# Kernel optimization log

Hardware: AMD Instinct MI355X
Metric: run time of the kernel (lower is better)

## Reference

```python
import jax, jax.numpy as jnp
import numpy as np

N_HEAD = 12
LN_EPS = 1e-5


def setup_inputs() -> dict:
    key = jax.random.key(0)
    ks = jax.random.split(key, 4)
    B, T, C = 4, 2048, 768
    s = C ** -0.5
    return {
        "x": jax.random.normal(ks[0], (B, T, C), jnp.float32),
        "w_attn": jax.random.normal(ks[1], (C, 3 * C), jnp.float32) * s,
        "b_attn": jnp.zeros((3 * C,), jnp.float32),
        "w_proj": jax.random.normal(ks[2], (C, C), jnp.float32) * s,
        "b_proj": jnp.zeros((C,), jnp.float32),
        "ln1_g": jnp.ones((C,), jnp.float32),
        "ln1_b": jnp.zeros((C,), jnp.float32),
        "ln2_g": jnp.ones((C,), jnp.float32),
        "ln2_b": jnp.zeros((C,), jnp.float32),
    }


def _layernorm(x, g, b):
    mu = jnp.mean(x, axis=-1, keepdims=True)
    var = jnp.mean(jnp.square(x - mu), axis=-1, keepdims=True)
    return (x - mu) * jax.lax.rsqrt(var + LN_EPS) * g + b


def _attn(h, w_attn, b_attn, w_proj, b_proj):
    B, T, C = h.shape
    hd = C // N_HEAD
    # Faithful to torch: view(B,T,H,3*hd) then split 3*hd -> q,k,v per head
    qkv = (h @ w_attn + b_attn).reshape(B, T, N_HEAD, 3, hd)
    q = jnp.transpose(qkv[:, :, :, 0, :], (0, 2, 1, 3))  # (B,H,T,hd)
    k = jnp.transpose(qkv[:, :, :, 1, :], (0, 2, 1, 3))
    v = jnp.transpose(qkv[:, :, :, 2, :], (0, 2, 1, 3))
    # NOTE: scale is C**-0.5 (full embed dim) and there is NO causal mask,
    # exactly as in the source.
    scores = jnp.einsum("bhtd,bhsd->bhts", q, k) * (C ** -0.5)
    a = jax.nn.softmax(scores, axis=-1)
    y = jnp.einsum("bhts,bhsd->bhtd", a, v)
    y = jnp.transpose(y, (0, 2, 1, 3)).reshape(B, T, C)
    return y @ w_proj + b_proj


def reference(x, w_attn, b_attn, w_proj, b_proj, ln1_g, ln1_b, ln2_g, ln2_b):
    # Faithful to source Block.forward: attn applied twice, MLP never called.
    x = x + _attn(_layernorm(x, ln1_g, ln1_b), w_attn, b_attn, w_proj, b_proj)
    x = x + _attn(_layernorm(x, ln2_g, ln2_b), w_attn, b_attn, w_proj, b_proj)
    return x
```

## Files before the change

### kernel.cpp

```cpp
#include <hip/hip_runtime.h>


using bf16x8 = __attribute__((ext_vector_type(8))) short;
using f32x4  = __attribute__((ext_vector_type(4))) float;
using f32x16 = __attribute__((ext_vector_type(16))) float;

__device__ __forceinline__ unsigned short f2b(float f) {
  unsigned u = __builtin_bit_cast(unsigned, f);
  u += 0x7FFFu + ((u >> 16) & 1u);
  return (unsigned short)(u >> 16);
}
__device__ __forceinline__ unsigned pk2(float a, float b) {
  unsigned ua = __builtin_bit_cast(unsigned, a);
  ua += 0x7FFFu + ((ua >> 16) & 1u);
  unsigned ub = __builtin_bit_cast(unsigned, b);
  ub += 0x7FFFu + ((ub >> 16) & 1u);
  return (ua >> 16) | (ub & 0xFFFF0000u);
}

__device__ __forceinline__ bf16x8 mk8(unsigned a, unsigned b, unsigned c,
                                      unsigned d) {
  union { unsigned u[4]; bf16x8 v; } x;
  x.u[0] = a; x.u[1] = b; x.u[2] = c; x.u[3] = d;
  return x.v;
}

#define ASYNC16(g, l)                                                        \
  __builtin_amdgcn_global_load_lds(                                          \
      (const __attribute__((address_space(1))) void*)(g),                    \
      (__attribute__((address_space(3))) void*)(l), 16, 0, 0)

#define PLSWAP(a, b) asm("v_permlane32_swap_b32 %0, %1" : "+v"(a), "+v"(b))

__global__ __launch_bounds__(256) void wt_kernel(const float* __restrict__ w,
                                                 unsigned short* __restrict__ wt,
                                                 int N) {
  __shared__ float tile[32][33];
  const int n0 = blockIdx.x * 32, k0 = blockIdx.y * 32;
  const int tx = threadIdx.x, ty = threadIdx.y;
#pragma unroll
  for (int i = 0; i < 32; i += 8)
    tile[ty + i][tx] = w[(size_t)(k0 + ty + i) * N + n0 + tx];
  __syncthreads();
#pragma unroll
  for (int i = 0; i < 32; i += 8)
    wt[(size_t)(n0 + ty + i) * 768 + k0 + tx] = f2b(tile[tx][ty + i]);
}

__global__ __launch_bounds__(256) void ln_kernel(const float* __restrict__ x,
                                                 const float* __restrict__ g,
                                                 const float* __restrict__ b,
                                                 unsigned short* __restrict__ h) {
  __shared__ float red[8];
  const int row = blockIdx.x;
  const int tid = threadIdx.x;
  const float* xr = x + (size_t)row * 768;
  float v0 = xr[tid], v1 = xr[tid + 256], v2 = xr[tid + 512];
  float s = v0 + v1 + v2;
  float s2 = v0 * v0 + v1 * v1 + v2 * v2;
#pragma unroll
  for (int off = 1; off < 64; off <<= 1) {
    s += __shfl_xor(s, off);
    s2 += __shfl_xor(s2, off);
  }
  if ((tid & 63) == 0) { red[tid >> 6] = s; red[4 + (tid >> 6)] = s2; }
  __syncthreads();
  const float S  = red[0] + red[1] + red[2] + red[3];
  const float S2 = red[4] + red[5] + red[6] + red[7];
  const float mu  = S * (1.0f / 768.0f);
  const float var = S2 * (1.0f / 768.0f) - mu * mu;
  const float inv = rsqrtf(var + 1e-5f);
  unsigned short* hr = h + (size_t)row * 768;
  hr[tid]       = f2b((v0 - mu) * inv * g[tid] + b[tid]);
  hr[tid + 256] = f2b((v1 - mu) * inv * g[tid + 256] + b[tid + 256]);
  hr[tid + 512] = f2b((v2 - mu) * inv * g[tid + 512] + b[tid + 512]);
}

template <int EPI>
__global__ __launch_bounds__(256, 2) void gemm_kernel(
    const unsigned short* __restrict__ A, const unsigned short* __restrict__ Bt,
    const float* __restrict__ bias, const float* __restrict__ resid,
    unsigned short* __restrict__ q, unsigned short* __restrict__ k,
    unsigned short* __restrict__ vt, float* __restrict__ outF) {
  __shared__ alignas(16) unsigned short As[128 * 32];
  __shared__ alignas(16) unsigned short Bs[128 * 32];

  const int tid = threadIdx.x;
  const int wv = tid >> 6;
  const int lane = tid & 63;
  const int quad = lane >> 4;
  const int l15 = lane & 15;
  const int m0 = blockIdx.y * 128;
  const int n0 = blockIdx.x * 128;

  const int o0 = wv * 1024 + lane * 16;
  const int rT0 = o0 >> 6, c0 = (o0 & 63) >> 1;
  const int o1 = o0 + 4096;
  const int rT1 = o1 >> 6, c1 = (o1 & 63) >> 1;

  const unsigned short* gA0 = A + (size_t)(m0 + rT0) * 768 + c0;
  const unsigned short* gA1 = A + (size_t)(m0 + rT1) * 768 + c1;
  const unsigned short* gB0 = Bt + (size_t)(n0 + rT0) * 768 + c0;
  const unsigned short* gB1 = Bt + (size_t)(n0 + rT1) * 768 + c1;
  unsigned short* lA0 = &As[wv * 512];
  unsigned short* lA1 = &As[wv * 512 + 2048];
  unsigned short* lB0 = &Bs[wv * 512];
  unsigned short* lB1 = &Bs[wv * 512 + 2048];

  f32x4 acc[4][4];
#pragma unroll
  for (int i = 0; i < 4; ++i)
#pragma unroll
    for (int j = 0; j < 4; ++j) acc[i][j] = {0.f, 0.f, 0.f, 0.f};

  const int mBase = (wv >> 1) * 64;
  const int nBase = (wv & 1) * 64;

  for (int kk = 0; kk < 24; ++kk) {
    const int ko = kk * 32;
    ASYNC16(gA0 + ko, lA0);
    ASYNC16(gA1 + ko, lA1);
    ASYNC16(gB0 + ko, lB0);
    ASYNC16(gB1 + ko, lB1);
    __syncthreads();
    bf16x8 af[4], bfv[4];
#pragma unroll
    for (int mt = 0; mt < 4; ++mt)
      af[mt] = *(const bf16x8*)&As[(mBase + mt * 16 + l15) * 32 + quad * 8];
#pragma unroll
    for (int nt = 0; nt < 4; ++nt)
      bfv[nt] = *(const bf16x8*)&Bs[(nBase + nt * 16 + l15) * 32 + quad * 8];
#pragma unroll
    for (int mt = 0; mt < 4; ++mt)
#pragma unroll
      for (int nt = 0; nt < 4; ++nt)
        acc[mt][nt] = __builtin_amdgcn_mfma_f32_16x16x32_bf16(af[mt], bfv[nt],
                                                              acc[mt][nt], 0, 0, 0);
    __syncthreads();
  }

  if constexpr (EPI == 0) {
    const float c2 = 0.052062786090587f;
#pragma unroll
    for (int mt = 0; mt < 4; ++mt) {
#pragma unroll
      for (int nt = 0; nt < 4; ++nt) {
        const int n = n0 + nBase + nt * 16 + l15;
        const int head = n / 192;
        const int rem = n - head * 192;
        const int sel = rem >> 6;
        const int d = rem & 63;
        const float bv = bias[n];
        const int mr = m0 + mBase + mt * 16 + quad * 4;
        const int bb = mr >> 11;
        const int t = mr & 2047;
        if (sel == 2) {
          const unsigned long long pk =
              (unsigned long long)pk2(acc[mt][nt][0] + bv, acc[mt][nt][1] + bv) |
              ((unsigned long long)pk2(acc[mt][nt][2] + bv, acc[mt][nt][3] + bv) << 32);
          *(unsigned long long*)&vt[(((size_t)bb * 12 + head) * 64 + d) * 2048 + t] = pk;
        } else {
          unsigned short* tgt = (sel == 0) ? q : k;
          const float sc = (sel == 0) ? c2 : 1.0f;
#pragma unroll
          for (int r = 0; r < 4; ++r)
            tgt[(((size_t)bb * 12 + head) * 2048 + t + r) * 64 + d] =
                f2b((acc[mt][nt][r] + bv) * sc);
        }
      }
    }
  } else {
#pragma unroll
    for (int mt = 0; mt < 4; ++mt) {
#pragma unroll
      for (int nt = 0; nt < 4; ++nt) {
        const int n = n0 + nBase + nt * 16 + l15;
        const float bv = bias[n];
#pragma unroll
        for (int r = 0; r < 4; ++r) {
          const int m = m0 + mBase + mt * 16 + quad * 4 + r;
          const size_t idx = (size_t)m * 768 + n;
          outF[idx] = resid[idx] + bv + acc[mt][nt][r];
        }
      }
    }
  }
}

__global__ __launch_bounds__(256, 3) void attn_kernel(
    const unsigned short* __restrict__ Q, const unsigned short* __restrict__ Km,
    const unsigned short* __restrict__ Vt, unsigned short* __restrict__ Y) {
  __shared__ alignas(16) unsigned short Ks[2][64 * 64];
  __shared__ alignas(16) unsigned short Vs[2][64 * 64];

  const int bh   = blockIdx.x;
  const int qt   = blockIdx.y;
  const int tid  = threadIdx.x;
  const int wv   = tid >> 6;
  const int lane = tid & 63;
  const int l31  = lane & 31;
  const int hi   = lane >> 5;
  const int s7   = l31 & 7;
  const size_t bhT = (size_t)bh * 2048;

  bf16x8 qf[4];
  {
    const unsigned short* qb =
        Q + (bhT + qt * 128 + wv * 32 + l31) * 64 + hi * 8;
#pragma unroll
    for (int ks = 0; ks < 4; ++ks) qf[ks] = *(const bf16x8*)(qb + ks * 16);
  }

  const int L0 = wv * 1024 + (lane << 4);
  const int L1 = L0 + 4096;
  const int r0 = L0 >> 7, b0 = (L0 & 127) ^ ((r0 & 7) << 4);
  const int r1 = L1 >> 7, b1 = (L1 & 127) ^ ((r1 & 7) << 4);
  const unsigned short* kg0 = Km + (bhT + r0) * 64 + (b0 >> 1);
  const unsigned short* kg1 = Km + (bhT + r1) * 64 + (b1 >> 1);
  const unsigned short* vg0 = Vt + ((size_t)bh * 64 + r0) * 2048 + (b0 >> 1);
  const unsigned short* vg1 = Vt + ((size_t)bh * 64 + r1) * 2048 + (b1 >> 1);
  const int kb0 = wv * 512, kb1 = wv * 512 + 2048;

  f32x16 o0, o1;
#pragma unroll
  for (int i = 0; i < 16; ++i) { o0[i] = 0.f; o1[i] = 0.f; }
  float l_acc = 0.f;

  ASYNC16(kg0, &Ks[0][kb0]);
  ASYNC16(kg1, &Ks[0][kb1]);
  ASYNC16(vg0, &Vs[0][kb0]);
  ASYNC16(vg1, &Vs[0][kb1]);
  __syncthreads();

  for (int c = 0; c < 32; ++c) {
    const int p = c & 1;
    if (c < 31) {
      const int ka = (c + 1) * 4096, va = (c + 1) * 64;
      ASYNC16(kg0 + ka, &Ks[p ^ 1][kb0]);
      ASYNC16(kg1 + ka, &Ks[p ^ 1][kb1]);
      ASYNC16(vg0 + va, &Vs[p ^ 1][kb0]);
      ASYNC16(vg1 + va, &Vs[p ^ 1][kb1]);
    }
    const unsigned short* Kp = &Ks[p][0];
    const unsigned short* Vp = &Vs[p][0];

#pragma unroll
    for (int tt = 0; tt < 2; ++tt) {
      f32x16 s;
#pragma unroll
      for (int i = 0; i < 16; ++i) s[i] = 0.f;
#pragma unroll
      for (int ks = 0; ks < 4; ++ks) {
        const int off = tt * 4096 + l31 * 128 + (((ks * 2 + hi) ^ s7) << 4);
        bf16x8 kf = *(const bf16x8*)&Kp[off >> 1];
        s = __builtin_amdgcn_mfma_f32_32x32x16_bf16(kf, qf[ks], s, 0, 0, 0);
      }

      unsigned dw[8];
      float lc = 0.f;
#pragma unroll
      for (int r2 = 0; r2 < 8; ++r2) {
        const float e0 = __builtin_amdgcn_exp2f(s[2 * r2]);
        const float e1 = __builtin_amdgcn_exp2f(s[2 * r2 + 1]);
        const unsigned u0 = __builtin_bit_cast(unsigned, e0) & 0xFFFF0000u;
        const unsigned u1 = __builtin_bit_cast(unsigned, e1) & 0xFFFF0000u;
        lc += __builtin_bit_cast(float, u0) + __builtin_bit_cast(float, u1);
        dw[r2] = (u0 >> 16) | u1;
      }
      l_acc += lc;

      PLSWAP(dw[0], dw[2]);
      PLSWAP(dw[1], dw[3]);
      PLSWAP(dw[4], dw[6]);
      PLSWAP(dw[5], dw[7]);
      const bf16x8 pf0 = mk8(dw[0], dw[1], dw[2], dw[3]);
      const bf16x8 pf1 = mk8(dw[4], dw[5], dw[6], dw[7]);

#pragma unroll
      for (int dt = 0; dt < 2; ++dt) {
        const int vb = dt * 4096 + l31 * 128;
        const int kv0 = tt * 2, kv1 = tt * 2 + 1;
        bf16x8 vf0 = *(const bf16x8*)&Vp[(vb + (((kv0 * 2 + hi) ^ s7) << 4)) >> 1];
        bf16x8 vf1 = *(const bf16x8*)&Vp[(vb + (((kv1 * 2 + hi) ^ s7) << 4)) >> 1];
        if (dt == 0) {
          o0 = __builtin_amdgcn_mfma_f32_32x32x16_bf16(vf0, pf0, o0, 0, 0, 0);
          o0 = __builtin_amdgcn_mfma_f32_32x32x16_bf16(vf1, pf1, o0, 0, 0, 0);
        } else {
          o1 = __builtin_amdgcn_mfma_f32_32x32x16_bf16(vf0, pf0, o1, 0, 0, 0);
          o1 = __builtin_amdgcn_mfma_f32_32x32x16_bf16(vf1, pf1, o1, 0, 0, 0);
        }
      }
    }
    __syncthreads();
  }

  unsigned la = __builtin_bit_cast(unsigned, l_acc), lb = la;
  PLSWAP(la, lb);
  const float l_tot =
      l_acc + __builtin_bit_cast(float, hi ? la : lb);
  const float rl = 1.0f / l_tot;

  const int b = bh / 12;
  const int head = bh - b * 12;
  const int row = qt * 128 + wv * 32 + l31;
  unsigned short* yb = Y + ((size_t)(b * 2048 + row)) * 768 + head * 64;
#pragma unroll
  for (int dt = 0; dt < 2; ++dt) {
#pragma unroll
    for (int g4 = 0; g4 < 4; ++g4) {
      const int d = dt * 32 + g4 * 8 + hi * 4;
      const float a0 = (dt ? o1[g4 * 4 + 0] : o0[g4 * 4 + 0]) * rl;
      const float a1 = (dt ? o1[g4 * 4 + 1] : o0[g4 * 4 + 1]) * rl;
      const float a2 = (dt ? o1[g4 * 4 + 2] : o0[g4 * 4 + 2]) * rl;
      const float a3 = (dt ? o1[g4 * 4 + 3] : o0[g4 * 4 + 3]) * rl;
      const unsigned long long pk =
          (unsigned long long)pk2(a0, a1) | ((unsigned long long)pk2(a2, a3) << 32);
      *(unsigned long long*)(yb + d) = pk;
    }
  }
}

extern "C" void kernel_launch(void* const* d_in, const int* in_sizes, int n_in,
                              void* d_out, int out_size, void* d_ws, size_t ws_size,
                              hipStream_t stream) {
  const float* x      = (const float*)d_in[0];
  const float* w_attn = (const float*)d_in[1];
  const float* b_attn = (const float*)d_in[2];
  const float* w_proj = (const float*)d_in[3];
  const float* b_proj = (const float*)d_in[4];
  const float* ln_g[2] = {(const float*)d_in[5], (const float*)d_in[7]};
  const float* ln_b[2] = {(const float*)d_in[6], (const float*)d_in[8]};
  float* out = (float*)d_out;

  unsigned short* wAt = (unsigned short*)d_ws;
  unsigned short* wPt = wAt + 2304 * 768;
  unsigned short* h   = wPt + 768 * 768;
  unsigned short* q   = h + 8192 * 768;
  unsigned short* k   = q + 48 * 2048 * 64;
  unsigned short* vt  = k + 48 * 2048 * 64;
  unsigned short* y   = vt + 48 * 2048 * 64;

  wt_kernel<<<dim3(72, 24), dim3(32, 8), 0, stream>>>(w_attn, wAt, 2304);
  wt_kernel<<<dim3(24, 24), dim3(32, 8), 0, stream>>>(w_proj, wPt, 768);

  for (int pass = 0; pass < 2; ++pass) {
    const float* xin = pass ? (const float*)out : x;
    ln_kernel<<<8192, 256, 0, stream>>>(xin, ln_g[pass], ln_b[pass], h);
    gemm_kernel<0><<<dim3(18, 64), 256, 0, stream>>>(h, wAt, b_attn, nullptr,
                                                     q, k, vt, nullptr);
    attn_kernel<<<dim3(48, 16), 256, 0, stream>>>(q, k, vt, y);
    gemm_kernel<1><<<dim3(6, 64), 256, 0, stream>>>(y, wPt, b_proj, xin,
                                                    nullptr, nullptr, nullptr, out);
  }
}
```

Measured before the change: 386.6 us.

## Give each attention wave 64 query rows and stage K/V via registers into padded LDS

The attention kernel now runs 128 threads per block, and each wave processes two 32-row query tiles, so every K and V fragment read from LDS feeds twice as many MFMAs. The direct-to-LDS async copies and XOR swizzle are replaced by global loads into registers, which are written to a padded LDS layout after compute to overlap with the math. MFMA sections are wrapped in s_setprio. This raises register pressure and halves the waves per block. The padded stride also leaves 16-byte LDS accesses only 8-byte aligned, which may cause bank conflicts or split accesses.

```diff
diff --git a/kernel.cpp b/kernel.cpp
--- a/kernel.cpp
+++ b/kernel.cpp
@@ -187,11 +187,12 @@
   }
 }
 
-__global__ __launch_bounds__(256, 3) void attn_kernel(
+#define KPAD 68
+__global__ __launch_bounds__(128, 2) void attn_kernel(
     const unsigned short* __restrict__ Q, const unsigned short* __restrict__ Km,
     const unsigned short* __restrict__ Vt, unsigned short* __restrict__ Y) {
-  __shared__ alignas(16) unsigned short Ks[2][64 * 64];
-  __shared__ alignas(16) unsigned short Vs[2][64 * 64];
+  __shared__ alignas(16) unsigned short Ks[2][64 * KPAD];
+  __shared__ alignas(16) unsigned short Vs[2][64 * KPAD];
 
   const int bh   = blockIdx.x;
   const int qt   = blockIdx.y;
@@ -200,122 +201,158 @@
   const int lane = tid & 63;
   const int l31  = lane & 31;
   const int hi   = lane >> 5;
-  const int s7   = l31 & 7;
   const size_t bhT = (size_t)bh * 2048;
 
-  bf16x8 qf[4];
+  bf16x8 qf0[4], qf1[4];
   {
-    const unsigned short* qb =
-        Q + (bhT + qt * 128 + wv * 32 + l31) * 64 + hi * 8;
-#pragma unroll
-    for (int ks = 0; ks < 4; ++ks) qf[ks] = *(const bf16x8*)(qb + ks * 16);
-  }
-
-  const int L0 = wv * 1024 + (lane << 4);
-  const int L1 = L0 + 4096;
-  const int r0 = L0 >> 7, b0 = (L0 & 127) ^ ((r0 & 7) << 4);
-  const int r1 = L1 >> 7, b1 = (L1 & 127) ^ ((r1 & 7) << 4);
-  const unsigned short* kg0 = Km + (bhT + r0) * 64 + (b0 >> 1);
-  const unsigned short* kg1 = Km + (bhT + r1) * 64 + (b1 >> 1);
-  const unsigned short* vg0 = Vt + ((size_t)bh * 64 + r0) * 2048 + (b0 >> 1);
-  const unsigned short* vg1 = Vt + ((size_t)bh * 64 + r1) * 2048 + (b1 >> 1);
-  const int kb0 = wv * 512, kb1 = wv * 512 + 2048;
-
-  f32x16 o0, o1;
-#pragma unroll
-  for (int i = 0; i < 16; ++i) { o0[i] = 0.f; o1[i] = 0.f; }
-  float l_acc = 0.f;
-
-  ASYNC16(kg0, &Ks[0][kb0]);
-  ASYNC16(kg1, &Ks[0][kb1]);
-  ASYNC16(vg0, &Vs[0][kb0]);
-  ASYNC16(vg1, &Vs[0][kb1]);
+    const unsigned short* qa =
+        Q + (bhT + qt * 128 + wv * 64 + l31) * 64 + hi * 8;
+#pragma unroll
+    for (int ks = 0; ks < 4; ++ks) {
+      qf0[ks] = *(const bf16x8*)(qa + ks * 16);
+      qf1[ks] = *(const bf16x8*)(qa + 32 * 64 + ks * 16);
+    }
+  }
+
+  const int sr = tid >> 1;
+  const int sh = tid & 1;
+  const unsigned short* gK = Km + (bhT + sr) * 64 + sh * 32;
+  const unsigned short* gV = Vt + ((size_t)bh * 64 + sr) * 2048 + sh * 32;
+  const int lofs = sr * KPAD + sh * 32;
+
+  f32x16 o00, o01, o10, o11;
+#pragma unroll
+  for (int i = 0; i < 16; ++i) { o00[i] = 0.f; o01[i] = 0.f; o10[i] = 0.f; o11[i] = 0.f; }
+  float l0 = 0.f, l1 = 0.f;
+
+  bf16x8 kst[4], vst[4];
+#pragma unroll
+  for (int i = 0; i < 4; ++i) {
+    kst[i] = *(const bf16x8*)(gK + i * 8);
+    vst[i] = *(const bf16x8*)(gV + i * 8);
+  }
+#pragma unroll
+  for (int i = 0; i < 4; ++i) {
+    *(bf16x8*)&Ks[0][lofs + i * 8] = kst[i];
+    *(bf16x8*)&Vs[0][lofs + i * 8] = vst[i];
+  }
   __syncthreads();
 
   for (int c = 0; c < 32; ++c) {
     const int p = c & 1;
     if (c < 31) {
-      const int ka = (c + 1) * 4096, va = (c + 1) * 64;
-      ASYNC16(kg0 + ka, &Ks[p ^ 1][kb0]);
-      ASYNC16(kg1 + ka, &Ks[p ^ 1][kb1]);
-      ASYNC16(vg0 + va, &Vs[p ^ 1][kb0]);
-      ASYNC16(vg1 + va, &Vs[p ^ 1][kb1]);
+      const unsigned short* gKn = gK + (size_t)(c + 1) * 4096;
+      const unsigned short* gVn = gV + (c + 1) * 64;
+#pragma unroll
+      for (int i = 0; i < 4; ++i) {
+        kst[i] = *(const bf16x8*)(gKn + i * 8);
+        vst[i] = *(const bf16x8*)(gVn + i * 8);
+      }
     }
     const unsigned short* Kp = &Ks[p][0];
     const unsigned short* Vp = &Vs[p][0];
 
 #pragma unroll
     for (int tt = 0; tt < 2; ++tt) {
-      f32x16 s;
-#pragma unroll
-      for (int i = 0; i < 16; ++i) s[i] = 0.f;
+      bf16x8 kf[4];
+#pragma unroll
+      for (int ks = 0; ks < 4; ++ks)
+        kf[ks] = *(const bf16x8*)&Kp[(tt * 32 + l31) * KPAD + ks * 16 + hi * 8];
+
+      f32x16 s0, s1;
+#pragma unroll
+      for (int i = 0; i < 16; ++i) { s0[i] = 0.f; s1[i] = 0.f; }
+      __builtin_amdgcn_s_setprio(1);
 #pragma unroll
       for (int ks = 0; ks < 4; ++ks) {
-        const int off = tt * 4096 + l31 * 128 + (((ks * 2 + hi) ^ s7) << 4);
-        bf16x8 kf = *(const bf16x8*)&Kp[off >> 1];
-        s = __builtin_amdgcn_mfma_f32_32x32x16_bf16(kf, qf[ks], s, 0, 0, 0);
-      }
-
-      unsigned dw[8];
-      float lc = 0.f;
-#pragma unroll
-      for (int r2 = 0; r2 < 8; ++r2) {
-        const float e0 = __builtin_amdgcn_exp2f(s[2 * r2]);
-        const float e1 = __builtin_amdgcn_exp2f(s[2 * r2 + 1]);
-        const unsigned u0 = __builtin_bit_cast(unsigned, e0) & 0xFFFF0000u;
-        const unsigned u1 = __builtin_bit_cast(unsigned, e1) & 0xFFFF0000u;
-        lc += __builtin_bit_cast(float, u0) + __builtin_bit_cast(float, u1);
-        dw[r2] = (u0 >> 16) | u1;
-      }
-      l_acc += lc;
-
-      PLSWAP(dw[0], dw[2]);
-      PLSWAP(dw[1], dw[3]);
-      PLSWAP(dw[4], dw[6]);
-      PLSWAP(dw[5], dw[7]);
-      const bf16x8 pf0 = mk8(dw[0], dw[1], dw[2], dw[3]);
-      const bf16x8 pf1 = mk8(dw[4], dw[5], dw[6], dw[7]);
-
-#pragma unroll
-      for (int dt = 0; dt < 2; ++dt) {
-        const int vb = dt * 4096 + l31 * 128;
-        const int kv0 = tt * 2, kv1 = tt * 2 + 1;
-        bf16x8 vf0 = *(const bf16x8*)&Vp[(vb + (((kv0 * 2 + hi) ^ s7) << 4)) >> 1];
-        bf16x8 vf1 = *(const bf16x8*)&Vp[(vb + (((kv1 * 2 + hi) ^ s7) << 4)) >> 1];
-        if (dt == 0) {
-          o0 = __builtin_amdgcn_mfma_f32_32x32x16_bf16(vf0, pf0, o0, 0, 0, 0);
-          o0 = __builtin_amdgcn_mfma_f32_32x32x16_bf16(vf1, pf1, o0, 0, 0, 0);
-        } else {
-          o1 = __builtin_amdgcn_mfma_f32_32x32x16_bf16(vf0, pf0, o1, 0, 0, 0);
-          o1 = __builtin_amdgcn_mfma_f32_32x32x16_bf16(vf1, pf1, o1, 0, 0, 0);
+        s0 = __builtin_amdgcn_mfma_f32_32x32x16_bf16(kf[ks], qf0[ks], s0, 0, 0, 0);
+        s1 = __builtin_amdgcn_mfma_f32_32x32x16_bf16(kf[ks], qf1[ks], s1, 0, 0, 0);
+      }
+      __builtin_amdgcn_s_setprio(0);
+
+      unsigned dwa[8], dwb[8];
+      {
+        float lc0 = 0.f, lc1 = 0.f;
+#pragma unroll
+        for (int r2 = 0; r2 < 8; ++r2) {
+          const float a0 = __builtin_amdgcn_exp2f(s0[2 * r2]);
+          const float a1 = __builtin_amdgcn_exp2f(s0[2 * r2 + 1]);
+          const unsigned ua0 = __builtin_bit_cast(unsigned, a0) & 0xFFFF0000u;
+          const unsigned ua1 = __builtin_bit_cast(unsigned, a1) & 0xFFFF0000u;
+          lc0 += __builtin_bit_cast(float, ua0) + __builtin_bit_cast(float, ua1);
+          dwa[r2] = (ua0 >> 16) | ua1;
+          const float b0 = __builtin_amdgcn_exp2f(s1[2 * r2]);
+          const float b1 = __builtin_amdgcn_exp2f(s1[2 * r2 + 1]);
+          const unsigned ub0 = __builtin_bit_cast(unsigned, b0) & 0xFFFF0000u;
+          const unsigned ub1 = __builtin_bit_cast(unsigned, b1) & 0xFFFF0000u;
+          lc1 += __builtin_bit_cast(float, ub0) + __builtin_bit_cast(float, ub1);
+          dwb[r2] = (ub0 >> 16) | ub1;
         }
+        l0 += lc0;
+        l1 += lc1;
+      }
+
+      PLSWAP(dwa[0], dwa[2]); PLSWAP(dwa[1], dwa[3]);
+      PLSWAP(dwa[4], dwa[6]); PLSWAP(dwa[5], dwa[7]);
+      PLSWAP(dwb[0], dwb[2]); PLSWAP(dwb[1], dwb[3]);
+      PLSWAP(dwb[4], dwb[6]); PLSWAP(dwb[5], dwb[7]);
+      const bf16x8 p0a = mk8(dwa[0], dwa[1], dwa[2], dwa[3]);
+      const bf16x8 p0b = mk8(dwa[4], dwa[5], dwa[6], dwa[7]);
+      const bf16x8 p1a = mk8(dwb[0], dwb[1], dwb[2], dwb[3]);
+      const bf16x8 p1b = mk8(dwb[4], dwb[5], dwb[6], dwb[7]);
+
+      bf16x8 v0a = *(const bf16x8*)&Vp[(l31) * KPAD + (tt * 2 + 0) * 16 + hi * 8];
+      bf16x8 v0b = *(const bf16x8*)&Vp[(l31) * KPAD + (tt * 2 + 1) * 16 + hi * 8];
+      bf16x8 v1a = *(const bf16x8*)&Vp[(32 + l31) * KPAD + (tt * 2 + 0) * 16 + hi * 8];
+      bf16x8 v1b = *(const bf16x8*)&Vp[(32 + l31) * KPAD + (tt * 2 + 1) * 16 + hi * 8];
+
+      __builtin_amdgcn_s_setprio(1);
+      o00 = __builtin_amdgcn_mfma_f32_32x32x16_bf16(v0a, p0a, o00, 0, 0, 0);
+      o00 = __builtin_amdgcn_mfma_f32_32x32x16_bf16(v0b, p0b, o00, 0, 0, 0);
+      o01 = __builtin_amdgcn_mfma_f32_32x32x16_bf16(v1a, p0a, o01, 0, 0, 0);
+      o01 = __builtin_amdgcn_mfma_f32_32x32x16_bf16(v1b, p0b, o01, 0, 0, 0);
+      o10 = __builtin_amdgcn_mfma_f32_32x32x16_bf16(v0a, p1a, o10, 0, 0, 0);
+      o10 = __builtin_amdgcn_mfma_f32_32x32x16_bf16(v0b, p1b, o10, 0, 0, 0);
+      o11 = __builtin_amdgcn_mfma_f32_32x32x16_bf16(v1a, p1a, o11, 0, 0, 0);
+      o11 = __builtin_amdgcn_mfma_f32_32x32x16_bf16(v1b, p1b, o11, 0, 0, 0);
+      __builtin_amdgcn_s_setprio(0);
+    }
+
+    if (c < 31) {
+#pragma unroll
+      for (int i = 0; i < 4; ++i) {
+        *(bf16x8*)&Ks[p ^ 1][lofs + i * 8] = kst[i];
+        *(bf16x8*)&Vs[p ^ 1][lofs + i * 8] = vst[i];
       }
     }
     __syncthreads();
   }
 
-  unsigned la = __builtin_bit_cast(unsigned, l_acc), lb = la;
-  PLSWAP(la, lb);
-  const float l_tot =
-      l_acc + __builtin_bit_cast(float, hi ? la : lb);
-  const float rl = 1.0f / l_tot;
+  unsigned la0 = __builtin_bit_cast(unsigned, l0), lb0 = la0;
+  PLSWAP(la0, lb0);
+  const float l0t = l0 + __builtin_bit_cast(float, hi ? la0 : lb0);
+  unsigned la1 = __builtin_bit_cast(unsigned, l1), lb1 = la1;
+  PLSWAP(la1, lb1);
+  const float l1t = l1 + __builtin_bit_cast(float, hi ? la1 : lb1);
 
   const int b = bh / 12;
   const int head = bh - b * 12;
-  const int row = qt * 128 + wv * 32 + l31;
-  unsigned short* yb = Y + ((size_t)(b * 2048 + row)) * 768 + head * 64;
-#pragma unroll
-  for (int dt = 0; dt < 2; ++dt) {
-#pragma unroll
-    for (int g4 = 0; g4 < 4; ++g4) {
-      const int d = dt * 32 + g4 * 8 + hi * 4;
-      const float a0 = (dt ? o1[g4 * 4 + 0] : o0[g4 * 4 + 0]) * rl;
-      const float a1 = (dt ? o1[g4 * 4 + 1] : o0[g4 * 4 + 1]) * rl;
-      const float a2 = (dt ? o1[g4 * 4 + 2] : o0[g4 * 4 + 2]) * rl;
-      const float a3 = (dt ? o1[g4 * 4 + 3] : o0[g4 * 4 + 3]) * rl;
-      const unsigned long long pk =
-          (unsigned long long)pk2(a0, a1) | ((unsigned long long)pk2(a2, a3) << 32);
-      *(unsigned long long*)(yb + d) = pk;
+#pragma unroll
+  for (int qs = 0; qs < 2; ++qs) {
+    const float rl = 1.0f / (qs ? l1t : l0t);
+    const int row = qt * 128 + wv * 64 + qs * 32 + l31;
+    unsigned short* yb = Y + ((size_t)(b * 2048 + row)) * 768 + head * 64;
+#pragma unroll
+    for (int dt = 0; dt < 2; ++dt) {
+      const f32x16& oo = qs ? (dt ? o11 : o10) : (dt ? o01 : o00);
+#pragma unroll
+      for (int g4 = 0; g4 < 4; ++g4) {
+        const int d = dt * 32 + g4 * 8 + hi * 4;
+        const unsigned long long pk =
+            (unsigned long long)pk2(oo[g4 * 4 + 0] * rl, oo[g4 * 4 + 1] * rl) |
+            ((unsigned long long)pk2(oo[g4 * 4 + 2] * rl, oo[g4 * 4 + 3] * rl) << 32);
+        *(unsigned long long*)(yb + d) = pk;
+      }
     }
   }
 }
@@ -348,7 +385,7 @@
     ln_kernel<<<8192, 256, 0, stream>>>(xin, ln_g[pass], ln_b[pass], h);
     gemm_kernel<0><<<dim3(18, 64), 256, 0, stream>>>(h, wAt, b_attn, nullptr,
                                                      q, k, vt, nullptr);
-    attn_kernel<<<dim3(48, 16), 256, 0, stream>>>(q, k, vt, y);
+    attn_kernel<<<dim3(48, 16), dim3(128), 0, stream>>>(q, k, vt, y);
     gemm_kernel<1><<<dim3(6, 64), 256, 0, stream>>>(y, wPt, b_proj, xin,
                                                     nullptr, nullptr, nullptr, out);
   }
```

Measured after the change: 459.4 us. 1.19x slower.
